# Kernel optimization log

Hardware: AMD Instinct MI355X
Metric: run time of the kernel (lower is better)

Reference implementation:

```python
import jax, jax.numpy as jnp
import numpy as np
import math

S, B, D = 2048, 2, 1024
H = 16
DH = D // H
WIN = 256
DIL = 1


def setup_inputs() -> dict:
    key = jax.random.key(0)
    ks = jax.random.split(key, 10)
    std = 1.0 / math.sqrt(D)
    return {
        "x": jax.random.normal(ks[0], (S, B, D), jnp.float32),
        "beta": jax.random.normal(ks[1], (H,), jnp.float32) * 0.02,
        "Wq": jax.random.normal(ks[2], (D, D), jnp.float32) * std,
        "bq": jnp.zeros((D,), jnp.float32),
        "Wk": jax.random.normal(ks[3], (D, D), jnp.float32) * std,
        "bk": jnp.zeros((D,), jnp.float32),
        "Wv": jax.random.normal(ks[4], (D, D), jnp.float32) * std,
        "bv": jnp.zeros((D,), jnp.float32),
        "Wo": jax.random.normal(ks[5], (D, D), jnp.float32) * std,
        "bo": jnp.zeros((D,), jnp.float32),
    }


def _split_heads(t):
    # (S, B, D) -> (B*H, S, DH), matching rearrange 's b (h d) -> (b h) s d'
    return t.reshape(S, B, H, DH).transpose(1, 2, 0, 3).reshape(B * H, S, DH)


def reference(x, beta, Wq, bq, Wk, bk, Wv, bv, Wo, bo):
    q = _split_heads(x @ Wq + bq)
    k = _split_heads(x @ Wk + bk)
    v = _split_heads(x @ Wv + bv)

    # per-head learnable temperature: q / (sqrt(d_head) * exp(beta))
    beta_exp = jnp.tile(jnp.exp(beta), B)  # (B*H,), head index = z % H
    q = q / (jnp.sqrt(jnp.asarray(DH, x.dtype)) * beta_exp)[:, None, None]

    # causal dilated windowed mask
    idx = jnp.arange(S)
    diff = idx[:, None] - idx[None, :]
    allowed = (diff >= 0) & (diff <= DIL * (WIN - 1)) & (diff % DIL == 0)
    mask = jnp.where(allowed, jnp.asarray(0.0, x.dtype), jnp.asarray(-jnp.inf, x.dtype))

    scores = jnp.einsum('zqd,zkd->zqk', q, k) + mask[None]
    # attention sink: extra zero-logit column absorbing probability mass
    scores = jnp.concatenate([scores, jnp.zeros((B * H, S, 1), scores.dtype)], axis=-1)
    attn = jax.nn.softmax(scores, axis=-1)[..., :-1]

    out = jnp.einsum('zqk,zkd->zqd', attn, v)
    # (B*H, S, DH) -> (S, B, D)
    out = out.reshape(B, H, S, DH).transpose(2, 0, 1, 3).reshape(S, B, D)
    return out @ Wo + bo
```

## Files before the change

### kernel.cpp

```cpp
#include <hip/hip_runtime.h>
#include <math.h>

#define S_LEN  2048
#define BATCH  2
#define DM     1024
#define NHEAD  16
#define DHEAD  64
#define WIN    256
#define MROWS  4096

#define KP   72
#define PPAD 68

typedef __attribute__((ext_vector_type(8))) short bf16x8;
typedef __attribute__((ext_vector_type(4))) float f32x4;

__device__ __forceinline__ unsigned short f2b(float f) {
    unsigned int u = __float_as_uint(f);
    return (unsigned short)((u + 0x7fffu + ((u >> 16) & 1u)) >> 16);
}
__device__ __forceinline__ void gld16(const void* g, void* l) {
    __builtin_amdgcn_global_load_lds(
        (const __attribute__((address_space(1))) void*)g,
        (__attribute__((address_space(3))) void*)l, 16, 0, 0);
}
__device__ __forceinline__ bf16x8 pack8(float4 a, float4 b) {
    bf16x8 r;
    r[0] = (short)f2b(a.x); r[1] = (short)f2b(a.y);
    r[2] = (short)f2b(a.z); r[3] = (short)f2b(a.w);
    r[4] = (short)f2b(b.x); r[5] = (short)f2b(b.y);
    r[6] = (short)f2b(b.z); r[7] = (short)f2b(b.w);
    return r;
}

__global__ __launch_bounds__(256)
void cvtx(const float* __restrict__ x, unsigned short* __restrict__ xb)
{
    const int i = (blockIdx.x * 256 + threadIdx.x) * 4;
    float4 f = *(const float4*)(x + i);
    ushort4 o; o.x = f2b(f.x); o.y = f2b(f.y); o.z = f2b(f.z); o.w = f2b(f.w);
    *(ushort4*)(xb + i) = o;
}

__global__ __launch_bounds__(256)
void twcvt4(const float* __restrict__ W0, const float* __restrict__ W1,
            const float* __restrict__ W2, const float* __restrict__ W3,
            unsigned short* __restrict__ T0, unsigned short* __restrict__ T1,
            unsigned short* __restrict__ T2, unsigned short* __restrict__ T3)
{
    const int zz = blockIdx.z;
    const float* W = (zz == 0) ? W0 : (zz == 1) ? W1 : (zz == 2) ? W2 : W3;
    unsigned short* WT = (zz == 0) ? T0 : (zz == 1) ? T1 : (zz == 2) ? T2 : T3;

    __shared__ float t32[32][33];
    const int bx = blockIdx.x * 32;
    const int by = blockIdx.y * 32;
    const int c  = threadIdx.x & 31;
    const int r0 = threadIdx.x >> 5;
#pragma unroll
    for (int p = 0; p < 4; ++p)
        t32[r0 + 8 * p][c] = W[(size_t)(by + r0 + 8 * p) * DM + bx + c];
    __syncthreads();
#pragma unroll
    for (int p = 0; p < 4; ++p)
        WT[(size_t)(bx + r0 + 8 * p) * DM + by + c] = f2b(t32[c][r0 + 8 * p]);
}

__global__ __launch_bounds__(256)
void gemm_qkv(const unsigned short* __restrict__ A,
              const unsigned short* __restrict__ BT,
              const float* __restrict__ b0,
              const float* __restrict__ b1,
              const float* __restrict__ b2,
              const float* __restrict__ beta,
              unsigned short* __restrict__ Cb)
{
    __shared__ unsigned short As[128 * 32];
    __shared__ unsigned short Bs[128 * 32];

    const int t  = threadIdx.x;
    const int wv = t >> 6, ln = t & 63;
    const int rowBase = blockIdx.y * 128;
    const int colBase = blockIdx.x * 128;

    const int m16 = ln & 15, g = ln >> 4;
    const int wr = wv >> 1, wc = wv & 1;
    const int swz = (m16 >> 1) & 3;

    const int lr = ln >> 2;
    const int lq = (ln & 3) ^ ((lr >> 1) & 3);
    const unsigned short* ga = A  + (size_t)(rowBase + wv * 16 + lr) * DM + lq * 8;
    const unsigned short* gb = BT + (size_t)(colBase + wv * 16 + lr) * DM + lq * 8;
    unsigned short* la0 = As + wv * 512;
    unsigned short* la1 = la0 + 2048;
    unsigned short* lb0 = Bs + wv * 512;
    unsigned short* lb1 = lb0 + 2048;

    f32x4 acc[4][4];
#pragma unroll
    for (int u = 0; u < 4; ++u)
#pragma unroll
        for (int v = 0; v < 4; ++v)
            acc[u][v] = (f32x4){0.f, 0.f, 0.f, 0.f};

    for (int kb = 0; kb < DM; kb += 32) {
        gld16(ga + kb, la0);
        gld16(ga + (size_t)64 * DM + kb, la1);
        gld16(gb + kb, lb0);
        gld16(gb + (size_t)64 * DM + kb, lb1);
        __syncthreads();

        bf16x8 af[4], bfr[4];
#pragma unroll
        for (int u = 0; u < 4; ++u)
            af[u] = *(const bf16x8*)&As[(wr * 64 + u * 16 + m16) * 32 + ((g ^ swz) * 8)];
#pragma unroll
        for (int v = 0; v < 4; ++v)
            bfr[v] = *(const bf16x8*)&Bs[(wc * 64 + v * 16 + m16) * 32 + ((g ^ swz) * 8)];
#pragma unroll
        for (int u = 0; u < 4; ++u)
#pragma unroll
            for (int v = 0; v < 4; ++v)
                acc[u][v] = __builtin_amdgcn_mfma_f32_16x16x32_bf16(
                    af[u], bfr[v], acc[u][v], 0, 0, 0);
        __syncthreads();
    }

    const int q4 = g * 4;
    const int sec = colBase >> 10;
    if (sec < 2) {
#pragma unroll
        for (int v = 0; v < 4; ++v) {
            const int col = colBase + wc * 64 + v * 16 + m16;
            const int h   = (col >> 6) & (NHEAD - 1);
            const int dh  = col & 63;
            const float bi = (sec == 0 ? b0 : b1)[col & (DM - 1)];
            const float sc = (sec == 0) ? 0.125f * __expf(-beta[h]) : 1.0f;
            unsigned short* base = Cb + (size_t)sec * MROWS * DM;
#pragma unroll
            for (int u = 0; u < 4; ++u)
#pragma unroll
                for (int r = 0; r < 4; ++r) {
                    const int row = rowBase + wr * 64 + u * 16 + q4 + r;
                    const int s = row >> 1, bb = row & 1;
                    const int z = bb * NHEAD + h;
                    base[((size_t)z * S_LEN + s) * DHEAD + dh] =
                        f2b((acc[u][v][r] + bi) * sc);
                }
        }
    } else {
        unsigned short* vtb = Cb + (size_t)2 * MROWS * DM;
#pragma unroll
        for (int v = 0; v < 4; ++v) {
            const int col = colBase + wc * 64 + v * 16 + m16;
            const int h   = (col >> 6) & (NHEAD - 1);
            const int dh  = col & 63;
            const float bi = b2[col & (DM - 1)];
#pragma unroll
            for (int u = 0; u < 4; ++u) {
                const int row0 = rowBase + wr * 64 + u * 16 + q4;
                const int s0   = row0 >> 1;
                ushort2 p0, p1;
                p0.x = f2b(acc[u][v][0] + bi);
                p0.y = f2b(acc[u][v][2] + bi);
                p1.x = f2b(acc[u][v][1] + bi);
                p1.y = f2b(acc[u][v][3] + bi);
                *(ushort2*)(vtb + ((size_t)(h * DHEAD + dh) * S_LEN + s0)) = p0;
                *(ushort2*)(vtb + ((size_t)((NHEAD + h) * DHEAD + dh) * S_LEN + s0)) = p1;
            }
        }
    }
}

__global__ __launch_bounds__(256)
void gemm_out(const unsigned short* __restrict__ A,
              const unsigned short* __restrict__ BT,
              const float* __restrict__ bias,
              float* __restrict__ Cf)
{
    __shared__ unsigned short As[128 * 32];
    __shared__ unsigned short Bs[64 * 32];

    const int t  = threadIdx.x;
    const int wv = t >> 6, ln = t & 63;
    const int rowBase = blockIdx.y * 128;
    const int colBase = blockIdx.x * 64;

    const int m16 = ln & 15, g = ln >> 4;
    const int wr = wv >> 1, wc = wv & 1;
    const int swz = (m16 >> 1) & 3;

    const int lr = ln >> 2;
    const int lq = (ln & 3) ^ ((lr >> 1) & 3);
    const unsigned short* ga = A  + (size_t)(rowBase + wv * 16 + lr) * DM + lq * 8;
    const unsigned short* gb = BT + (size_t)(colBase + wv * 16 + lr) * DM + lq * 8;
    unsigned short* la0 = As + wv * 512;
    unsigned short* la1 = la0 + 2048;
    unsigned short* lb  = Bs + wv * 512;

    f32x4 acc[4][2];
#pragma unroll
    for (int u = 0; u < 4; ++u)
#pragma unroll
        for (int v = 0; v < 2; ++v)
            acc[u][v] = (f32x4){0.f, 0.f, 0.f, 0.f};

    for (int kb = 0; kb < DM; kb += 32) {
        gld16(ga + kb, la0);
        gld16(ga + (size_t)64 * DM + kb, la1);
        gld16(gb + kb, lb);
        __syncthreads();

        bf16x8 af[4], bfr[2];
#pragma unroll
        for (int u = 0; u < 4; ++u)
            af[u] = *(const bf16x8*)&As[(wr * 64 + u * 16 + m16) * 32 + ((g ^ swz) * 8)];
#pragma unroll
        for (int v = 0; v < 2; ++v)
            bfr[v] = *(const bf16x8*)&Bs[(wc * 32 + v * 16 + m16) * 32 + ((g ^ swz) * 8)];
#pragma unroll
        for (int u = 0; u < 4; ++u)
#pragma unroll
            for (int v = 0; v < 2; ++v)
                acc[u][v] = __builtin_amdgcn_mfma_f32_16x16x32_bf16(
                    af[u], bfr[v], acc[u][v], 0, 0, 0);
        __syncthreads();
    }

    const int q4 = g * 4;
#pragma unroll
    for (int v = 0; v < 2; ++v) {
        const int col = colBase + wc * 32 + v * 16 + m16;
        const float bi = bias[col];
#pragma unroll
        for (int u = 0; u < 4; ++u)
#pragma unroll
            for (int r = 0; r < 4; ++r) {
                const int row = rowBase + wr * 64 + u * 16 + q4 + r;
                Cf[(size_t)row * DM + col] = acc[u][v][r] + bi;
            }
    }
}

__global__ __launch_bounds__(256, 4)
void attn_mfma(const unsigned short* __restrict__ q,
               const unsigned short* __restrict__ k,
               const unsigned short* __restrict__ vt,
               unsigned short* __restrict__ ao)
{
    __shared__ unsigned short Ks[64 * KP];
    __shared__ unsigned short Vs[64 * KP];
    __shared__ float Ps[64][PPAD];

    const int t   = threadIdx.x;
    const int wv  = t >> 6, ln = t & 63;
    const int m16 = ln & 15, g = ln >> 4;
    const int z   = blockIdx.y;
    const int q0  = blockIdx.x * 64;
    const size_t zbase = (size_t)z * S_LEN * DHEAD;

    const unsigned short* qrow = q + zbase + (size_t)(q0 + wv * 16 + m16) * DHEAD;
    bf16x8 qf0 = *(const bf16x8*)(qrow + g * 8);
    bf16x8 qf1 = *(const bf16x8*)(qrow + 32 + g * 8);

    f32x4 oacc[4];
#pragma unroll
    for (int v4 = 0; v4 < 4; ++v4) oacc[v4] = (f32x4){0.f, 0.f, 0.f, 0.f};
    float lr[4];
#pragma unroll
    for (int r = 0; r < 4; ++r) lr[r] = 1.f;

    for (int c = 0; c < 5; ++c) {
        const int kb = q0 - 256 + c * 64;
        if (kb < 0) continue;
        __syncthreads();

#pragma unroll
        for (int i = 0; i < 2; ++i) {
            const int id  = t + 256 * i;
            const int row = id >> 3;
            const int co  = (id & 7) * 8;
            *(bf16x8*)&Ks[row * KP + co] =
                *(const bf16x8*)(k + zbase + (size_t)(kb + row) * DHEAD + co);
            *(bf16x8*)&Vs[row * KP + co] =
                *(const bf16x8*)(vt + ((size_t)z * DHEAD + row) * S_LEN + kb + co);
        }
        __syncthreads();

        f32x4 sacc[4];
#pragma unroll
        for (int v4 = 0; v4 < 4; ++v4) {
            sacc[v4] = (f32x4){0.f, 0.f, 0.f, 0.f};
            bf16x8 kf0 = *(const bf16x8*)&Ks[(v4 * 16 + m16) * KP + g * 8];
            sacc[v4] = __builtin_amdgcn_mfma_f32_16x16x32_bf16(qf0, kf0, sacc[v4], 0, 0, 0);
            bf16x8 kf1 = *(const bf16x8*)&Ks[(v4 * 16 + m16) * KP + 32 + g * 8];
            sacc[v4] = __builtin_amdgcn_mfma_f32_16x16x32_bf16(qf1, kf1, sacc[v4], 0, 0, 0);
        }

        const bool mhi = (c == 4), mlo = (c == 0);
#pragma unroll
        for (int r = 0; r < 4; ++r) {
            const int ig = q0 + wv * 16 + g * 4 + r;
            float rsum = 0.f;
#pragma unroll
            for (int v4 = 0; v4 < 4; ++v4) {
                const int jg = kb + v4 * 16 + m16;
                float x = sacc[v4][r];
                const bool valid = (!mhi || jg <= ig) && (!mlo || jg >= ig - (WIN - 1));
                x = valid ? x : -1e30f;
                const float pp = __expf(x);
                Ps[wv * 16 + g * 4 + r][v4 * 16 + m16] = pp;
                rsum += pp;
            }
#pragma unroll
            for (int off = 1; off < 16; off <<= 1)
                rsum += __shfl_xor(rsum, off, 64);
            lr[r] += rsum;
        }
        __syncthreads();

        const float* prow = &Ps[wv * 16 + m16][0];
        bf16x8 pf0 = pack8(*(const float4*)(prow + g * 8),
                           *(const float4*)(prow + g * 8 + 4));
        bf16x8 pf1 = pack8(*(const float4*)(prow + 32 + g * 8),
                           *(const float4*)(prow + 32 + g * 8 + 4));
#pragma unroll
        for (int v4 = 0; v4 < 4; ++v4) {
            bf16x8 vf0 = *(const bf16x8*)&Vs[(v4 * 16 + m16) * KP + g * 8];
            oacc[v4] = __builtin_amdgcn_mfma_f32_16x16x32_bf16(pf0, vf0, oacc[v4], 0, 0, 0);
            bf16x8 vf1 = *(const bf16x8*)&Vs[(v4 * 16 + m16) * KP + 32 + g * 8];
            oacc[v4] = __builtin_amdgcn_mfma_f32_16x16x32_bf16(pf1, vf1, oacc[v4], 0, 0, 0);
        }
    }

    const int bb = z >> 4, h = z & 15;
#pragma unroll
    for (int r = 0; r < 4; ++r) {
        const int ig  = q0 + wv * 16 + g * 4 + r;
        const float inv = 1.f / lr[r];
#pragma unroll
        for (int v4 = 0; v4 < 4; ++v4)
            ao[(size_t)(ig * BATCH + bb) * DM + h * DHEAD + v4 * 16 + m16] =
                f2b(oacc[v4][r] * inv);
    }
}

extern "C" void kernel_launch(void* const* d_in, const int* in_sizes, int n_in,
                              void* d_out, int out_size, void* d_ws, size_t ws_size,
                              hipStream_t stream)
{
    const float* x    = (const float*)d_in[0];
    const float* beta = (const float*)d_in[1];
    const float* Wq   = (const float*)d_in[2];
    const float* bq   = (const float*)d_in[3];
    const float* Wk   = (const float*)d_in[4];
    const float* bk   = (const float*)d_in[5];
    const float* Wv   = (const float*)d_in[6];
    const float* bv   = (const float*)d_in[7];
    const float* Wo   = (const float*)d_in[8];
    const float* bo   = (const float*)d_in[9];
    float* out = (float*)d_out;

    unsigned short* w = (unsigned short*)d_ws;
    const size_t seg = (size_t)MROWS * DM;
    unsigned short* qb  = w;
    unsigned short* kb  = w + seg;
    unsigned short* vtb = w + 2 * seg;
    unsigned short* ab  = w + 3 * seg;
    unsigned short* xb  = w + 4 * seg;
    unsigned short* wtq = w + 5 * seg;
    unsigned short* wtk = wtq + (size_t)DM * DM;
    unsigned short* wtv = wtk + (size_t)DM * DM;
    unsigned short* wto = wtv + (size_t)DM * DM;

    cvtx<<<4096, 256, 0, stream>>>(x, xb);
    twcvt4<<<dim3(32, 32, 4), 256, 0, stream>>>(Wq, Wk, Wv, Wo, wtq, wtk, wtv, wto);

    gemm_qkv<<<dim3(3072 / 128, MROWS / 128), 256, 0, stream>>>(
        xb, wtq, bq, bk, bv, beta, qb);

    attn_mfma<<<dim3(S_LEN / 64, BATCH * NHEAD), 256, 0, stream>>>(qb, kb, vtb, ab);

    gemm_out<<<dim3(DM / 64, MROWS / 128), 256, 0, stream>>>(ab, wto, bo, out);
}
```

Measured before the change: 185.0 us.

## Rewrite QKV GEMM with 256x192 tiles, double-buffered LDS and interleaved prefetch

```diff
diff --git a/kernel.cpp b/kernel.cpp
--- a/kernel.cpp
+++ b/kernel.cpp
@@ -12,6 +12,10 @@
 #define KP   72
 #define PPAD 68
 
+#define BM 256
+#define BN 192
+#define BK 64
+
 typedef __attribute__((ext_vector_type(8))) short bf16x8;
 typedef __attribute__((ext_vector_type(4))) float f32x4;
 
@@ -66,7 +70,7 @@
         WT[(size_t)(bx + r0 + 8 * p) * DM + by + c] = f2b(t32[c][r0 + 8 * p]);
 }
 
-__global__ __launch_bounds__(256)
+__global__ __launch_bounds__(512, 2)
 void gemm_qkv(const unsigned short* __restrict__ A,
               const unsigned short* __restrict__ BT,
               const float* __restrict__ b0,
@@ -75,90 +79,195 @@
               const float* __restrict__ beta,
               unsigned short* __restrict__ Cb)
 {
-    __shared__ unsigned short As[128 * 32];
-    __shared__ unsigned short Bs[128 * 32];
-
-    const int t  = threadIdx.x;
-    const int wv = t >> 6, ln = t & 63;
-    const int rowBase = blockIdx.y * 128;
-    const int colBase = blockIdx.x * 128;
-
-    const int m16 = ln & 15, g = ln >> 4;
-    const int wr = wv >> 1, wc = wv & 1;
-    const int swz = (m16 >> 1) & 3;
-
-    const int lr = ln >> 2;
-    const int lq = (ln & 3) ^ ((lr >> 1) & 3);
-    const unsigned short* ga = A  + (size_t)(rowBase + wv * 16 + lr) * DM + lq * 8;
-    const unsigned short* gb = BT + (size_t)(colBase + wv * 16 + lr) * DM + lq * 8;
-    unsigned short* la0 = As + wv * 512;
-    unsigned short* la1 = la0 + 2048;
-    unsigned short* lb0 = Bs + wv * 512;
-    unsigned short* lb1 = lb0 + 2048;
-
-    f32x4 acc[4][4];
-#pragma unroll
-    for (int u = 0; u < 4; ++u)
-#pragma unroll
-        for (int v = 0; v < 4; ++v)
+    __shared__ unsigned short Ab[2][BM * BK];
+    __shared__ unsigned short Bb[2][BN * BK];
+
+    const int t   = threadIdx.x;
+    const int ln  = t & 63;
+    const int wv  = t >> 6;
+    const int wr  = wv >> 2;
+    const int wc  = wv & 3;
+    const int m16 = ln & 15;
+    const int g   = ln >> 4;
+    const int sw  = m16 & 7;
+
+    const int rowBase = blockIdx.y * BM;
+    const int colBase = blockIdx.x * BN;
+
+    const int sr  = t >> 3;
+    const int scx = (t & 7) ^ (sr & 7);
+    const size_t gOff = (size_t)sr * DM + scx * 8;
+    const int    ldOff = t * 8;
+
+    f32x4 acc[8][3];
+#pragma unroll
+    for (int u = 0; u < 8; ++u)
+#pragma unroll
+        for (int v = 0; v < 3; ++v)
             acc[u][v] = (f32x4){0.f, 0.f, 0.f, 0.f};
 
-    for (int kb = 0; kb < DM; kb += 32) {
-        gld16(ga + kb, la0);
-        gld16(ga + (size_t)64 * DM + kb, la1);
-        gld16(gb + kb, lb0);
-        gld16(gb + (size_t)64 * DM + kb, lb1);
-        __syncthreads();
-
-        bf16x8 af[4], bfr[4];
+    {
+        const unsigned short* a0 = A  + (size_t)rowBase * DM + gOff;
+        const unsigned short* bt = BT + (size_t)colBase * DM + gOff;
+#pragma unroll
+        for (int cb = 0; cb < 3; ++cb)
+            gld16(bt + (size_t)cb * 64 * DM, &Bb[0][cb * 4096 + ldOff]);
+#pragma unroll
+        for (int ca = 0; ca < 4; ++ca)
+            gld16(a0 + (size_t)ca * 64 * DM, &Ab[0][ca * 4096 + ldOff]);
+        asm volatile("s_waitcnt vmcnt(0)" ::: "memory");
+        __builtin_amdgcn_s_barrier();
+    }
+
+    bf16x8 af[4][2], bfr[2][2];
+
+    for (int kt = 0; kt < DM / BK; ++kt) {
+        const int cur = kt & 1;
+        const unsigned short* Ac = Ab[cur];
+        const unsigned short* Bc = Bb[cur];
+        unsigned short* An = Ab[cur ^ 1];
+        unsigned short* Bn = Bb[cur ^ 1];
+        const bool hn = (kt < DM / BK - 1);
+        const unsigned short* aS = A  + (size_t)rowBase * DM + (kt + 1) * BK + gOff;
+        const unsigned short* bS = BT + (size_t)colBase * DM + (kt + 1) * BK + gOff;
+
+#pragma unroll
+        for (int u = 0; u < 4; ++u) {
+            const int ro = (wr * 128 + u * 16 + m16) * BK;
+#pragma unroll
+            for (int kk = 0; kk < 2; ++kk)
+                af[u][kk] = *(const bf16x8*)&Ac[ro + (((kk << 2) | g) ^ sw) * 8];
+        }
+#pragma unroll
+        for (int v = 0; v < 2; ++v) {
+            const int ro = (wc * 48 + v * 16 + m16) * BK;
+#pragma unroll
+            for (int kk = 0; kk < 2; ++kk)
+                bfr[v][kk] = *(const bf16x8*)&Bc[ro + (((kk << 2) | g) ^ sw) * 8];
+        }
+        if (hn) {
+            gld16(bS,                      &Bn[ldOff]);
+            gld16(bS + (size_t)64 * DM,    &Bn[4096 + ldOff]);
+        }
+        __builtin_amdgcn_s_barrier();
+        __builtin_amdgcn_s_setprio(1);
 #pragma unroll
         for (int u = 0; u < 4; ++u)
-            af[u] = *(const bf16x8*)&As[(wr * 64 + u * 16 + m16) * 32 + ((g ^ swz) * 8)];
-#pragma unroll
-        for (int v = 0; v < 4; ++v)
-            bfr[v] = *(const bf16x8*)&Bs[(wc * 64 + v * 16 + m16) * 32 + ((g ^ swz) * 8)];
+#pragma unroll
+            for (int v = 0; v < 2; ++v) {
+                acc[u][v] = __builtin_amdgcn_mfma_f32_16x16x32_bf16(
+                    af[u][0], bfr[v][0], acc[u][v], 0, 0, 0);
+                acc[u][v] = __builtin_amdgcn_mfma_f32_16x16x32_bf16(
+                    af[u][1], bfr[v][1], acc[u][v], 0, 0, 0);
+            }
+        __builtin_amdgcn_s_setprio(0);
+        __builtin_amdgcn_s_barrier();
+
+        {
+            const int ro = (wc * 48 + 32 + m16) * BK;
+#pragma unroll
+            for (int kk = 0; kk < 2; ++kk)
+                bfr[0][kk] = *(const bf16x8*)&Bc[ro + (((kk << 2) | g) ^ sw) * 8];
+        }
+        if (hn) {
+            gld16(bS + (size_t)128 * DM,   &Bn[2 * 4096 + ldOff]);
+            gld16(aS,                      &An[ldOff]);
+        }
+        __builtin_amdgcn_s_barrier();
+        __builtin_amdgcn_s_setprio(1);
+#pragma unroll
+        for (int u = 0; u < 4; ++u) {
+            acc[u][2] = __builtin_amdgcn_mfma_f32_16x16x32_bf16(
+                af[u][0], bfr[0][0], acc[u][2], 0, 0, 0);
+            acc[u][2] = __builtin_amdgcn_mfma_f32_16x16x32_bf16(
+                af[u][1], bfr[0][1], acc[u][2], 0, 0, 0);
+        }
+        __builtin_amdgcn_s_setprio(0);
+        asm volatile("s_waitcnt vmcnt(4)" ::: "memory");
+        __builtin_amdgcn_s_barrier();
+
+#pragma unroll
+        for (int u = 0; u < 4; ++u) {
+            const int ro = (wr * 128 + 64 + u * 16 + m16) * BK;
+#pragma unroll
+            for (int kk = 0; kk < 2; ++kk)
+                af[u][kk] = *(const bf16x8*)&Ac[ro + (((kk << 2) | g) ^ sw) * 8];
+        }
+#pragma unroll
+        for (int v = 0; v < 2; ++v) {
+            const int ro = (wc * 48 + v * 16 + m16) * BK;
+#pragma unroll
+            for (int kk = 0; kk < 2; ++kk)
+                bfr[v][kk] = *(const bf16x8*)&Bc[ro + (((kk << 2) | g) ^ sw) * 8];
+        }
+        if (hn) {
+            gld16(aS + (size_t)128 * DM,   &An[2 * 4096 + ldOff]);
+            gld16(aS + (size_t)64 * DM,    &An[4096 + ldOff]);
+        }
+        __builtin_amdgcn_s_barrier();
+        __builtin_amdgcn_s_setprio(1);
 #pragma unroll
         for (int u = 0; u < 4; ++u)
 #pragma unroll
-            for (int v = 0; v < 4; ++v)
-                acc[u][v] = __builtin_amdgcn_mfma_f32_16x16x32_bf16(
-                    af[u], bfr[v], acc[u][v], 0, 0, 0);
-        __syncthreads();
+            for (int v = 0; v < 2; ++v) {
+                acc[4 + u][v] = __builtin_amdgcn_mfma_f32_16x16x32_bf16(
+                    af[u][0], bfr[v][0], acc[4 + u][v], 0, 0, 0);
+                acc[4 + u][v] = __builtin_amdgcn_mfma_f32_16x16x32_bf16(
+                    af[u][1], bfr[v][1], acc[4 + u][v], 0, 0, 0);
+            }
+        __builtin_amdgcn_s_setprio(0);
+        __builtin_amdgcn_s_barrier();
+
+        {
+            const int ro = (wc * 48 + 32 + m16) * BK;
+#pragma unroll
+            for (int kk = 0; kk < 2; ++kk)
+                bfr[0][kk] = *(const bf16x8*)&Bc[ro + (((kk << 2) | g) ^ sw) * 8];
+        }
+        if (hn) {
+            gld16(aS + (size_t)192 * DM,   &An[3 * 4096 + ldOff]);
+        }
+        __builtin_amdgcn_s_barrier();
+        __builtin_amdgcn_s_setprio(1);
+#pragma unroll
+        for (int u = 0; u < 4; ++u) {
+            acc[4 + u][2] = __builtin_amdgcn_mfma_f32_16x16x32_bf16(
+                af[u][0], bfr[0][0], acc[4 + u][2], 0, 0, 0);
+            acc[4 + u][2] = __builtin_amdgcn_mfma_f32_16x16x32_bf16(
+                af[u][1], bfr[0][1], acc[4 + u][2], 0, 0, 0);
+        }
+        __builtin_amdgcn_s_setprio(0);
+        asm volatile("s_waitcnt vmcnt(2)" ::: "memory");
+        __builtin_amdgcn_s_barrier();
     }
 
     const int q4 = g * 4;
-    const int sec = colBase >> 10;
-    if (sec < 2) {
-#pragma unroll
-        for (int v = 0; v < 4; ++v) {
-            const int col = colBase + wc * 64 + v * 16 + m16;
-            const int h   = (col >> 6) & (NHEAD - 1);
-            const int dh  = col & 63;
+#pragma unroll
+    for (int v = 0; v < 3; ++v) {
+        const int col = colBase + wc * 48 + v * 16 + m16;
+        const int sec = col >> 10;
+        const int h   = (col >> 6) & (NHEAD - 1);
+        const int dh  = col & 63;
+        if (sec < 2) {
             const float bi = (sec == 0 ? b0 : b1)[col & (DM - 1)];
             const float sc = (sec == 0) ? 0.125f * __expf(-beta[h]) : 1.0f;
             unsigned short* base = Cb + (size_t)sec * MROWS * DM;
 #pragma unroll
-            for (int u = 0; u < 4; ++u)
+            for (int u = 0; u < 8; ++u)
 #pragma unroll
                 for (int r = 0; r < 4; ++r) {
-                    const int row = rowBase + wr * 64 + u * 16 + q4 + r;
+                    const int row = rowBase + wr * 128 + u * 16 + q4 + r;
                     const int s = row >> 1, bb = row & 1;
                     const int z = bb * NHEAD + h;
                     base[((size_t)z * S_LEN + s) * DHEAD + dh] =
                         f2b((acc[u][v][r] + bi) * sc);
                 }
-        }
-    } else {
-        unsigned short* vtb = Cb + (size_t)2 * MROWS * DM;
-#pragma unroll
-        for (int v = 0; v < 4; ++v) {
-            const int col = colBase + wc * 64 + v * 16 + m16;
-            const int h   = (col >> 6) & (NHEAD - 1);
-            const int dh  = col & 63;
+        } else {
+            unsigned short* vtb = Cb + (size_t)2 * MROWS * DM;
             const float bi = b2[col & (DM - 1)];
 #pragma unroll
-            for (int u = 0; u < 4; ++u) {
-                const int row0 = rowBase + wr * 64 + u * 16 + q4;
+            for (int u = 0; u < 8; ++u) {
+                const int row0 = rowBase + wr * 128 + u * 16 + q4;
                 const int s0   = row0 >> 1;
                 ushort2 p0, p1;
                 p0.x = f2b(acc[u][v][0] + bi);
@@ -376,7 +485,7 @@
     cvtx<<<4096, 256, 0, stream>>>(x, xb);
     twcvt4<<<dim3(32, 32, 4), 256, 0, stream>>>(Wq, Wk, Wv, Wo, wtq, wtk, wtv, wto);
 
-    gemm_qkv<<<dim3(3072 / 128, MROWS / 128), 256, 0, stream>>>(
+    gemm_qkv<<<dim3(3072 / BN, MROWS / BM), 512, 0, stream>>>(
         xb, wtq, bq, bk, bv, beta, qb);
 
     attn_mfma<<<dim3(S_LEN / 64, BATCH * NHEAD), 256, 0, stream>>>(qb, kb, vtb, ab);
```

Result: faster. 175.2 us (-5.3%).
